# Optimization experiments

Measured on AMD Instinct MI355X. Metric: run time of the kernel, lower is better.

Reference implementation:

```python
import jax, jax.numpy as jnp
import numpy as np

B, IN_DIM, HID, E, G, EPS = 8192, 1024, 2048, 16, 256, 1e-5

def setup_inputs() -> dict:
    key = jax.random.key(0)
    ks = jax.random.split(key, 8)
    s = 0.02
    f32 = jnp.float32
    return {
        "x": jax.random.normal(ks[0], (B, IN_DIM), f32),
        "g_ln_w": jnp.ones((IN_DIM,), f32),
        "g_ln_b": jnp.zeros((IN_DIM,), f32),
        "g_w1": jax.random.normal(ks[1], (IN_DIM, G), f32) * s,
        "g_b1": jnp.zeros((G,), f32),
        "g_w2": jax.random.normal(ks[2], (G, E), f32) * s,
        "g_b2": jnp.zeros((E,), f32),
        "e_ln_w": jnp.ones((E, IN_DIM), f32),
        "e_ln_b": jnp.zeros((E, IN_DIM), f32),
        "e_w1": jax.random.normal(ks[3], (E, IN_DIM, HID), f32) * s,
        "e_b1": jnp.zeros((E, HID), f32),
        "e_w2": jax.random.normal(ks[4], (E, HID, G), f32) * s,
        "e_b2": jnp.zeros((E, G), f32),
        "e_w3": jax.random.normal(ks[5], (E, G, 2), f32) * s,
        "e_b3": jnp.zeros((E, 2), f32),
    }

def reference(x, g_ln_w, g_ln_b, g_w1, g_b1, g_w2, g_b2,
              e_ln_w, e_ln_b, e_w1, e_b1, e_w2, e_b2, e_w3, e_b3):
    # Shared normalization (all LayerNorms normalize the same x), per-module affine.
    mu = jnp.mean(x, axis=-1, keepdims=True)
    var = jnp.mean((x - mu) ** 2, axis=-1, keepdims=True)
    xhat = (x - mu) * jax.lax.rsqrt(var + EPS)            # [B, D]
    # Gate: LN -> Linear(256) -> ReLU -> Linear(E) -> softmax
    gh = jax.nn.relu((xhat * g_ln_w + g_ln_b) @ g_w1 + g_b1)
    gate_w = jax.nn.softmax(gh @ g_w2 + g_b2, axis=-1)    # [B, E]
    # All experts batched over leading E axis (dropout = identity in eval)
    xe = xhat[None] * e_ln_w[:, None, :] + e_ln_b[:, None, :]              # [E, B, D]
    h1 = jax.nn.relu(jnp.einsum('ebd,edh->ebh', xe, e_w1) + e_b1[:, None, :])  # [E, B, HID]
    h2 = jax.nn.relu(jnp.einsum('ebh,ehg->ebg', h1, e_w2) + e_b2[:, None, :])  # [E, B, G]
    oe = jnp.einsum('ebg,ego->ebo', h2, e_w3) + e_b3[:, None, :]               # [E, B, 2]
    out = jnp.einsum('ebo,be->bo', oe, gate_w)                                  # [B, 2]
    pred_mean = out[:, 0:1]
    pred_var = jax.nn.softplus(out[:, 1:2]) + 1e-6
    return (pred_mean, pred_var)
```

## Files before the change

### kernel.cpp

```cpp
#include <hip/hip_runtime.h>

#define B_ 8192
#define D_ 1024
#define H_ 2048
#define E_ 16
#define G_ 256

typedef unsigned short u16;
typedef __attribute__((ext_vector_type(4))) float f32x4;
typedef __attribute__((ext_vector_type(8))) short bf16x8;
typedef __attribute__((ext_vector_type(4))) unsigned short u16x4;

__device__ u16   g_W1t[(size_t)E_ * H_ * D_];
__device__ u16   g_W2t[(size_t)E_ * G_ * H_];
__device__ u16   g_GW1t[(size_t)G_ * D_];
__device__ u16   g_xhat[(size_t)B_ * D_];
__device__ u16   g_gh[(size_t)B_ * G_];
__device__ float g_b1part[4 * E_ * H_];
__device__ float g_b1p[E_ * H_];
__device__ float g_gb1part[4 * G_];
__device__ float g_gb1p[G_];
__device__ float g_gate[(size_t)B_ * E_];
__device__ float g_oep[(size_t)E_ * B_ * 2];

__device__ __forceinline__ u16 f2bf(float f) {
  unsigned int u = __float_as_uint(f);
  unsigned int r = (u + 0x7fffu + ((u >> 16) & 1u)) >> 16;
  return (u16)r;
}
__device__ __forceinline__ float bf2f(u16 u) {
  return __uint_as_float((unsigned int)u << 16);
}
__device__ __forceinline__ void gld16(const void* g, void* l) {
  __builtin_amdgcn_global_load_lds(
      (const __attribute__((address_space(1))) unsigned int*)g,
      (__attribute__((address_space(3))) unsigned int*)l, 16, 0, 0);
}

__global__ __launch_bounds__(256) void k_transpose_scale(
    const float* __restrict__ src, const float* __restrict__ scale,
    int which, int R, int C) {
  u16* dstb = (which == 0) ? g_W1t : (which == 1) ? g_W2t : g_GW1t;
  __shared__ float tile[32][33];
  int z = blockIdx.z;
  const float* s = src + (size_t)z * R * C;
  u16* d = dstb + (size_t)z * R * C;
  int c0 = blockIdx.x * 32, r0 = blockIdx.y * 32;
#pragma unroll
  for (int i = 0; i < 4; i++) {
    int r = r0 + threadIdx.y + i * 8;
    int c = c0 + threadIdx.x;
    float v = s[(size_t)r * C + c];
    if (scale) v *= scale[(size_t)z * R + r];
    tile[threadIdx.y + i * 8][threadIdx.x] = v;
  }
  __syncthreads();
#pragma unroll
  for (int i = 0; i < 4; i++) {
    int c = c0 + threadIdx.y + i * 8;
    int r = r0 + threadIdx.x;
    d[(size_t)c * R + r] = f2bf(tile[threadIdx.x][threadIdx.y + i * 8]);
  }
}

__global__ __launch_bounds__(256) void k_prep_bias(
    const float* __restrict__ W, const float* __restrict__ lnb,
    const float* __restrict__ bias, int which, int D, int N, int Z) {
  float* part = (which == 0) ? g_b1part : g_gb1part;
  int z = blockIdx.x;
  int n = blockIdx.y * 256 + threadIdx.x;
  int dc = blockIdx.z;
  int dlen = D / 4, d0 = dc * dlen;
  const float* Wb = W + (size_t)z * D * N;
  const float* lb = lnb + (size_t)z * D;
  float acc = (dc == 0) ? bias[(size_t)z * N + n] : 0.f;
  for (int d = d0; d < d0 + dlen; d++) acc += lb[d] * Wb[(size_t)d * N + n];
  part[((size_t)dc * Z + z) * N + n] = acc;
}

__global__ __launch_bounds__(256) void k_combine_bias(int which, int len) {
  const float* part = (which == 0) ? g_b1part : g_gb1part;
  float* out = (which == 0) ? g_b1p : g_gb1p;
  int i = blockIdx.x * 256 + threadIdx.x;
  if (i < len)
    out[i] = part[i] + part[len + i] + part[2 * len + i] + part[3 * len + i];
}

__global__ __launch_bounds__(256) void k_layernorm(const float* __restrict__ x) {
  int row = blockIdx.x;
  int tid = threadIdx.x;
  const float4 v = ((const float4*)(x + (size_t)row * D_))[tid];
  float s1 = v.x + v.y + v.z + v.w;
  float s2 = v.x * v.x + v.y * v.y + v.z * v.z + v.w * v.w;
#pragma unroll
  for (int m = 1; m < 64; m <<= 1) {
    s1 += __shfl_xor(s1, m, 64);
    s2 += __shfl_xor(s2, m, 64);
  }
  __shared__ float red[8];
  int w = tid >> 6, l = tid & 63;
  if (l == 0) { red[w * 2] = s1; red[w * 2 + 1] = s2; }
  __syncthreads();
  s1 = red[0] + red[2] + red[4] + red[6];
  s2 = red[1] + red[3] + red[5] + red[7];
  float mu = s1 * (1.f / D_);
  float var = s2 * (1.f / D_) - mu * mu;
  float rs = rsqrtf(var + 1e-5f);
  u16x4 p;
  p.x = f2bf((v.x - mu) * rs);
  p.y = f2bf((v.y - mu) * rs);
  p.z = f2bf((v.z - mu) * rs);
  p.w = f2bf((v.w - mu) * rs);
  ((u16x4*)(g_xhat + (size_t)row * D_))[tid] = p;
}

__global__ __launch_bounds__(256) void k_gating_gemm() {
  __shared__ alignas(16) char pool[8192 + 16384];
  u16* A_st = (u16*)pool;
  u16* B_st = (u16*)(pool + 8192);
  const int r0 = blockIdx.x * 64;
  const int n0 = blockIdx.y * 128;
  const int tid = threadIdx.x, l = tid & 63, w = tid >> 6;
  const int l15 = l & 15, l4 = l >> 4;
  const int srow = tid >> 3, sk8 = tid & 7;

  f32x4 zero4 = {0.f, 0.f, 0.f, 0.f};
  f32x4 acc[4][2];
#pragma unroll
  for (int i = 0; i < 4; i++)
#pragma unroll
    for (int j = 0; j < 2; j++) acc[i][j] = zero4;

  for (int s = 0; s < 16; s++) {
    __syncthreads();
#pragma unroll
    for (int r = 0; r < 2; r++) {
      int row = r * 32 + srow;
      gld16(g_xhat + (size_t)(r0 + row) * D_ + s * 64 + sk8 * 8,
            (char*)A_st + (r * 256 + (tid & 192)) * 16);
    }
#pragma unroll
    for (int r = 0; r < 4; r++) {
      int row = r * 32 + srow;
      gld16(g_GW1t + (size_t)(n0 + row) * D_ + s * 64 + sk8 * 8,
            (char*)B_st + (r * 256 + (tid & 192)) * 16);
    }
    __syncthreads();
#pragma unroll
    for (int t = 0; t < 2; t++) {
      bf16x8 af[4], bfr[2];
#pragma unroll
      for (int mi = 0; mi < 4; mi++)
        af[mi] = *(const bf16x8*)&A_st[(mi * 16 + l15) * 64 + t * 32 + l4 * 8];
#pragma unroll
      for (int ni = 0; ni < 2; ni++)
        bfr[ni] = *(const bf16x8*)&B_st[(w * 32 + ni * 16 + l15) * 64 + t * 32 + l4 * 8];
#pragma unroll
      for (int mi = 0; mi < 4; mi++)
#pragma unroll
        for (int ni = 0; ni < 2; ni++)
          acc[mi][ni] = __builtin_amdgcn_mfma_f32_16x16x32_bf16(
              af[mi], bfr[ni], acc[mi][ni], 0, 0, 0);
    }
  }
#pragma unroll
  for (int ni = 0; ni < 2; ni++) {
    int n = n0 + w * 32 + ni * 16 + l15;
    float bv = g_gb1p[n];
#pragma unroll
    for (int mi = 0; mi < 4; mi++)
#pragma unroll
      for (int q = 0; q < 4; q++) {
        int row = r0 + mi * 16 + l4 * 4 + q;
        g_gh[(size_t)row * G_ + n] = f2bf(fmaxf(acc[mi][ni][q] + bv, 0.f));
      }
  }
}

__global__ __launch_bounds__(256) void k_gating_softmax(
    const float* __restrict__ gw2, const float* __restrict__ gb2) {
  int tid = threadIdx.x;
  int rl = tid >> 4, j = tid & 15;
  int row = blockIdx.x * 16 + rl;
  const u16* gr = g_gh + (size_t)row * G_;
  float acc = gb2[j];
  for (int k = 0; k < G_; k++) acc += bf2f(gr[k]) * gw2[k * 16 + j];
  float m = acc;
#pragma unroll
  for (int mm = 1; mm < 16; mm <<= 1) m = fmaxf(m, __shfl_xor(m, mm, 64));
  float e = expf(acc - m);
  float s = e;
#pragma unroll
  for (int mm = 1; mm < 16; mm <<= 1) s += __shfl_xor(s, mm, 64);
  g_gate[(size_t)row * 16 + j] = e / s;
}

__global__ __launch_bounds__(256, 2) void k_chain(
    const float* __restrict__ eb2,
    const float* __restrict__ w3,
    const float* __restrict__ b3)
{
  constexpr int BM = 128, NT = 128, BK = 64;
  constexpr int C1LD = NT + 8;
  __shared__ alignas(16) char pool[32768 + BM * C1LD * 2 + 2 * BM * 2 * 4];
  u16* A_st = (u16*)pool;
  u16* B_st = (u16*)(pool + 16384);
  u16* C1 = (u16*)(pool + 32768);
  float* oeac = (float*)(pool + 32768 + BM * C1LD * 2);

  const int wg = blockIdx.x;
  const int xcd = wg & 7;
  const int idx = wg >> 3;
  const int e = xcd * 2 + (idx >> 6);
  const int r0 = (idx & 63) * BM;

  const int tid = threadIdx.x;
  const int l = tid & 63, w = tid >> 6;
  const int wr = w >> 1, wc = w & 1;
  const int l15 = l & 15, l4 = l >> 4;
  const int srow = tid >> 3, sk8 = tid & 7;

  const u16* W1e = g_W1t + (size_t)e * H_ * D_;
  const u16* W2e = g_W2t + (size_t)e * G_ * H_;

  f32x4 zero4 = {0.f, 0.f, 0.f, 0.f};
  f32x4 acc2[4][8];
#pragma unroll
  for (int i = 0; i < 4; i++)
#pragma unroll
    for (int j = 0; j < 8; j++) acc2[i][j] = zero4;

  for (int kk = 0; kk < H_ / NT; kk++) {
    f32x4 acc1[4][4];
#pragma unroll
    for (int i = 0; i < 4; i++)
#pragma unroll
      for (int j = 0; j < 4; j++) acc1[i][j] = zero4;

    for (int s = 0; s < D_ / BK; s++) {
      __syncthreads();
#pragma unroll
      for (int r = 0; r < 4; r++) {
        int row = r * 32 + srow;
        gld16(g_xhat + (size_t)(r0 + row) * D_ + s * BK + sk8 * 8,
              (char*)A_st + (r * 256 + (tid & 192)) * 16);
      }
#pragma unroll
      for (int r = 0; r < 4; r++) {
        int row = r * 32 + srow;
        gld16(W1e + (size_t)(kk * NT + row) * D_ + s * BK + sk8 * 8,
              (char*)B_st + (r * 256 + (tid & 192)) * 16);
      }
      __syncthreads();
#pragma unroll
      for (int t = 0; t < 2; t++) {
        bf16x8 af[4], bfr[4];
#pragma unroll
        for (int mi = 0; mi < 4; mi++)
          af[mi] = *(const bf16x8*)&A_st[(wr * 64 + mi * 16 + l15) * BK + t * 32 + l4 * 8];
#pragma unroll
        for (int ni = 0; ni < 4; ni++)
          bfr[ni] = *(const bf16x8*)&B_st[(wc * 64 + ni * 16 + l15) * BK + t * 32 + l4 * 8];
#pragma unroll
        for (int mi = 0; mi < 4; mi++)
#pragma unroll
          for (int ni = 0; ni < 4; ni++)
            acc1[mi][ni] = __builtin_amdgcn_mfma_f32_16x16x32_bf16(
                af[mi], bfr[ni], acc1[mi][ni], 0, 0, 0);
      }
    }
    float bn[4];
#pragma unroll
    for (int ni = 0; ni < 4; ni++)
      bn[ni] = g_b1p[e * H_ + kk * NT + wc * 64 + ni * 16 + l15];
#pragma unroll
    for (int mi = 0; mi < 4; mi++)
#pragma unroll
      for (int ni = 0; ni < 4; ni++)
#pragma unroll
        for (int q = 0; q < 4; q++) {
          float v = fmaxf(acc1[mi][ni][q] + bn[ni], 0.f);
          C1[(wr * 64 + mi * 16 + l4 * 4 + q) * C1LD + wc * 64 + ni * 16 + l15] = f2bf(v);
        }
    __syncthreads();

#pragma unroll
    for (int k2 = 0; k2 < 2; k2++) {
#pragma unroll
      for (int r = 0; r < 8; r++) {
        int grow = r * 32 + srow;
        gld16(W2e + (size_t)grow * H_ + kk * NT + k2 * 64 + sk8 * 8,
              pool + (r * 256 + (tid & 192)) * 16);
      }
      __syncthreads();
      const u16* B2 = (const u16*)pool;
#pragma unroll
      for (int t = 0; t < 2; t++) {
        bf16x8 a2[4];
#pragma unroll
        for (int mi = 0; mi < 4; mi++)
          a2[mi] = *(const bf16x8*)&C1[(wr * 64 + mi * 16 + l15) * C1LD + k2 * 64 + t * 32 + l4 * 8];
#pragma unroll
        for (int nj = 0; nj < 8; nj++) {
          bf16x8 b2 = *(const bf16x8*)&B2[(wc * 128 + nj * 16 + l15) * 64 + t * 32 + l4 * 8];
#pragma unroll
          for (int mi = 0; mi < 4; mi++)
            acc2[mi][nj] = __builtin_amdgcn_mfma_f32_16x16x32_bf16(
                a2[mi], b2, acc2[mi][nj], 0, 0, 0);
        }
      }
      __syncthreads();
    }
  }

  float w30[8], w31[8], bb[8];
#pragma unroll
  for (int nj = 0; nj < 8; nj++) {
    int g = wc * 128 + nj * 16 + l15;
    w30[nj] = w3[(e * G_ + g) * 2 + 0];
    w31[nj] = w3[(e * G_ + g) * 2 + 1];
    bb[nj] = eb2[e * G_ + g];
  }
#pragma unroll
  for (int mi = 0; mi < 4; mi++)
#pragma unroll
    for (int q = 0; q < 4; q++) {
      float s0 = 0.f, s1 = 0.f;
#pragma unroll
      for (int nj = 0; nj < 8; nj++) {
        float h = fmaxf(acc2[mi][nj][q] + bb[nj], 0.f);
        s0 += h * w30[nj];
        s1 += h * w31[nj];
      }
#pragma unroll
      for (int mm = 1; mm < 16; mm <<= 1) {
        s0 += __shfl_xor(s0, mm, 64);
        s1 += __shfl_xor(s1, mm, 64);
      }
      if (l15 == 0) {
        int row = wr * 64 + mi * 16 + l4 * 4 + q;
        oeac[(wc * BM + row) * 2 + 0] = s0;
        oeac[(wc * BM + row) * 2 + 1] = s1;
      }
    }
  __syncthreads();
  if (tid < BM) {
    int row = tid;
    float gg = g_gate[(size_t)(r0 + row) * E_ + e];
    float o0 = oeac[row * 2 + 0] + oeac[(BM + row) * 2 + 0] + b3[e * 2 + 0];
    float o1 = oeac[row * 2 + 1] + oeac[(BM + row) * 2 + 1] + b3[e * 2 + 1];
    g_oep[((size_t)e * B_ + (r0 + row)) * 2 + 0] = gg * o0;
    g_oep[((size_t)e * B_ + (r0 + row)) * 2 + 1] = gg * o1;
  }
}

__global__ __launch_bounds__(256) void k_finalize(float* __restrict__ out) {
  int i = blockIdx.x * 256 + threadIdx.x;
  float m = 0.f, v = 0.f;
#pragma unroll
  for (int e = 0; e < E_; e++) {
    m += g_oep[((size_t)e * B_ + i) * 2 + 0];
    v += g_oep[((size_t)e * B_ + i) * 2 + 1];
  }
  float sp = (v > 20.f) ? v : log1pf(expf(v));
  out[i] = m;
  out[B_ + i] = sp + 1e-6f;
}

extern "C" void kernel_launch(void* const* d_in, const int* in_sizes, int n_in,
                              void* d_out, int out_size, void* d_ws, size_t ws_size,
                              hipStream_t stream) {
  const float* x    = (const float*)d_in[0];
  const float* glnw = (const float*)d_in[1];
  const float* glnb = (const float*)d_in[2];
  const float* gw1  = (const float*)d_in[3];
  const float* gb1  = (const float*)d_in[4];
  const float* gw2  = (const float*)d_in[5];
  const float* gb2  = (const float*)d_in[6];
  const float* elnw = (const float*)d_in[7];
  const float* elnb = (const float*)d_in[8];
  const float* ew1  = (const float*)d_in[9];
  const float* eb1  = (const float*)d_in[10];
  const float* ew2  = (const float*)d_in[11];
  const float* eb2  = (const float*)d_in[12];
  const float* ew3  = (const float*)d_in[13];
  const float* eb3  = (const float*)d_in[14];
  float* out = (float*)d_out;
  (void)d_ws; (void)ws_size;

  dim3 tb(32, 8);
  k_transpose_scale<<<dim3(H_ / 32, D_ / 32, E_), tb, 0, stream>>>(ew1, elnw, 0, D_, H_);
  k_transpose_scale<<<dim3(G_ / 32, H_ / 32, E_), tb, 0, stream>>>(ew2, nullptr, 1, H_, G_);
  k_transpose_scale<<<dim3(G_ / 32, D_ / 32, 1), tb, 0, stream>>>(gw1, glnw, 2, D_, G_);

  k_prep_bias<<<dim3(E_, H_ / 256, 4), 256, 0, stream>>>(ew1, elnb, eb1, 0, D_, H_, E_);
  k_prep_bias<<<dim3(1, 1, 4), 256, 0, stream>>>(gw1, glnb, gb1, 1, D_, G_, 1);
  k_combine_bias<<<(E_ * H_ + 255) / 256, 256, 0, stream>>>(0, E_ * H_);
  k_combine_bias<<<1, 256, 0, stream>>>(1, G_);

  k_layernorm<<<B_, 256, 0, stream>>>(x);
  k_gating_gemm<<<dim3(B_ / 64, G_ / 128), 256, 0, stream>>>();
  k_gating_softmax<<<B_ / 16, 256, 0, stream>>>(gw2, gb2);

  k_chain<<<dim3(B_ / 128 * E_), 256, 0, stream>>>(eb2, ew3, eb3);

  k_finalize<<<B_ / 256, 256, 0, stream>>>(out);
}
```

Measured before the change: 1.539 ms.

## XOR-swizzle LDS tiles and regroup chain workgroups by expert across XCDs

```diff
diff --git a/kernel.cpp b/kernel.cpp
--- a/kernel.cpp
+++ b/kernel.cpp
@@ -121,8 +121,9 @@
   const int r0 = blockIdx.x * 64;
   const int n0 = blockIdx.y * 128;
   const int tid = threadIdx.x, l = tid & 63, w = tid >> 6;
-  const int l15 = l & 15, l4 = l >> 4;
-  const int srow = tid >> 3, sk8 = tid & 7;
+  const int l15 = l & 15, l4 = l >> 4, lx = l15 & 7;
+  const int srow = tid >> 3;
+  const int sk8s = (tid & 7) ^ ((tid >> 3) & 7);
 
   f32x4 zero4 = {0.f, 0.f, 0.f, 0.f};
   f32x4 acc[4][2];
@@ -136,13 +137,13 @@
 #pragma unroll
     for (int r = 0; r < 2; r++) {
       int row = r * 32 + srow;
-      gld16(g_xhat + (size_t)(r0 + row) * D_ + s * 64 + sk8 * 8,
+      gld16(g_xhat + (size_t)(r0 + row) * D_ + s * 64 + sk8s * 8,
             (char*)A_st + (r * 256 + (tid & 192)) * 16);
     }
 #pragma unroll
     for (int r = 0; r < 4; r++) {
       int row = r * 32 + srow;
-      gld16(g_GW1t + (size_t)(n0 + row) * D_ + s * 64 + sk8 * 8,
+      gld16(g_GW1t + (size_t)(n0 + row) * D_ + s * 64 + sk8s * 8,
             (char*)B_st + (r * 256 + (tid & 192)) * 16);
     }
     __syncthreads();
@@ -151,10 +152,10 @@
       bf16x8 af[4], bfr[2];
 #pragma unroll
       for (int mi = 0; mi < 4; mi++)
-        af[mi] = *(const bf16x8*)&A_st[(mi * 16 + l15) * 64 + t * 32 + l4 * 8];
+        af[mi] = *(const bf16x8*)&A_st[(mi * 16 + l15) * 64 + ((t * 4 + l4) ^ lx) * 8];
 #pragma unroll
       for (int ni = 0; ni < 2; ni++)
-        bfr[ni] = *(const bf16x8*)&B_st[(w * 32 + ni * 16 + l15) * 64 + t * 32 + l4 * 8];
+        bfr[ni] = *(const bf16x8*)&B_st[(w * 32 + ni * 16 + l15) * 64 + ((t * 4 + l4) ^ lx) * 8];
 #pragma unroll
       for (int mi = 0; mi < 4; mi++)
 #pragma unroll
@@ -211,14 +212,15 @@
   const int wg = blockIdx.x;
   const int xcd = wg & 7;
   const int idx = wg >> 3;
-  const int e = xcd * 2 + (idx >> 6);
-  const int r0 = (idx & 63) * BM;
+  const int e = idx >> 3;
+  const int r0 = (xcd * 8 + (idx & 7)) * BM;
 
   const int tid = threadIdx.x;
   const int l = tid & 63, w = tid >> 6;
   const int wr = w >> 1, wc = w & 1;
-  const int l15 = l & 15, l4 = l >> 4;
-  const int srow = tid >> 3, sk8 = tid & 7;
+  const int l15 = l & 15, l4 = l >> 4, lx = l15 & 7;
+  const int srow = tid >> 3;
+  const int sk8s = (tid & 7) ^ ((tid >> 3) & 7);
 
   const u16* W1e = g_W1t + (size_t)e * H_ * D_;
   const u16* W2e = g_W2t + (size_t)e * G_ * H_;
@@ -242,13 +244,13 @@
 #pragma unroll
       for (int r = 0; r < 4; r++) {
         int row = r * 32 + srow;
-        gld16(g_xhat + (size_t)(r0 + row) * D_ + s * BK + sk8 * 8,
+        gld16(g_xhat + (size_t)(r0 + row) * D_ + s * BK + sk8s * 8,
               (char*)A_st + (r * 256 + (tid & 192)) * 16);
       }
 #pragma unroll
       for (int r = 0; r < 4; r++) {
         int row = r * 32 + srow;
-        gld16(W1e + (size_t)(kk * NT + row) * D_ + s * BK + sk8 * 8,
+        gld16(W1e + (size_t)(kk * NT + row) * D_ + s * BK + sk8s * 8,
               (char*)B_st + (r * 256 + (tid & 192)) * 16);
       }
       __syncthreads();
@@ -257,10 +259,10 @@
         bf16x8 af[4], bfr[4];
 #pragma unroll
         for (int mi = 0; mi < 4; mi++)
-          af[mi] = *(const bf16x8*)&A_st[(wr * 64 + mi * 16 + l15) * BK + t * 32 + l4 * 8];
+          af[mi] = *(const bf16x8*)&A_st[(wr * 64 + mi * 16 + l15) * BK + ((t * 4 + l4) ^ lx) * 8];
 #pragma unroll
         for (int ni = 0; ni < 4; ni++)
-          bfr[ni] = *(const bf16x8*)&B_st[(wc * 64 + ni * 16 + l15) * BK + t * 32 + l4 * 8];
+          bfr[ni] = *(const bf16x8*)&B_st[(wc * 64 + ni * 16 + l15) * BK + ((t * 4 + l4) ^ lx) * 8];
 #pragma unroll
         for (int mi = 0; mi < 4; mi++)
 #pragma unroll
@@ -289,7 +291,7 @@
 #pragma unroll
       for (int r = 0; r < 8; r++) {
         int grow = r * 32 + srow;
-        gld16(W2e + (size_t)grow * H_ + kk * NT + k2 * 64 + sk8 * 8,
+        gld16(W2e + (size_t)grow * H_ + kk * NT + k2 * 64 + sk8s * 8,
               pool + (r * 256 + (tid & 192)) * 16);
       }
       __syncthreads();
@@ -302,7 +304,7 @@
           a2[mi] = *(const bf16x8*)&C1[(wr * 64 + mi * 16 + l15) * C1LD + k2 * 64 + t * 32 + l4 * 8];
 #pragma unroll
         for (int nj = 0; nj < 8; nj++) {
-          bf16x8 b2 = *(const bf16x8*)&B2[(wc * 128 + nj * 16 + l15) * 64 + t * 32 + l4 * 8];
+          bf16x8 b2 = *(const bf16x8*)&B2[(wc * 128 + nj * 16 + l15) * 64 + ((t * 4 + l4) ^ lx) * 8];
 #pragma unroll
           for (int mi = 0; mi < 4; mi++)
             acc2[mi][nj] = __builtin_amdgcn_mfma_f32_16x16x32_bf16(
```

Result: faster. 1.341 ms (-12.8%).
